# Performance work log

Hardware: AMD Instinct MI355X
Metric: run time of the kernel (lower is better)

Reference implementation:

```python
import jax, jax.numpy as jnp
import numpy as np

N_NODES = 100000


def _sage_conv(x, src, dst, W_l, b_l, W_r):
    # mean-aggregate neighbor (source) features at target nodes
    gathered = x[src]                                   # [E, D]
    summed = jax.ops.segment_sum(gathered, dst, num_segments=N_NODES)  # [N, D]
    deg = jax.ops.segment_sum(jnp.ones((src.shape[0],), x.dtype), dst,
                              num_segments=N_NODES)     # [N]
    mean = summed / jnp.maximum(deg, 1.0)[:, None]      # zero stays zero for isolated nodes
    # PyG SAGEConv: lin_l(aggr) + lin_r(x); bias on lin_l only
    return mean @ W_l + b_l + x @ W_r


def setup_inputs() -> dict:
    key = jax.random.key(0)
    ks = jax.random.split(key, 9)
    x = jax.random.normal(ks[0], (N_NODES, 128), dtype=jnp.float32)
    edge_index = jax.random.randint(ks[1], (2, 1600000), 0, N_NODES, dtype=jnp.int64)
    s1 = 1.0 / np.sqrt(128.0)
    s2 = 1.0 / np.sqrt(32.0)
    return {
        "x": x,
        "edge_index": edge_index,
        "W1_l": jax.random.normal(ks[2], (128, 32), jnp.float32) * s1,
        "b1_l": jax.random.normal(ks[3], (32,), jnp.float32) * s1,
        "W1_r": jax.random.normal(ks[4], (128, 32), jnp.float32) * s1,
        "W2_l": jax.random.normal(ks[5], (32, 32), jnp.float32) * s2,
        "b2_l": jax.random.normal(ks[6], (32,), jnp.float32) * s2,
        "W2_r": jax.random.normal(ks[7], (32, 32), jnp.float32) * s2,
    }


def reference(x, edge_index, W1_l, b1_l, W1_r, W2_l, b2_l, W2_r):
    src, dst = edge_index[0], edge_index[1]
    h = _sage_conv(x, src, dst, W1_l, b1_l, W1_r)
    h = jax.nn.relu(h)
    # dropout is identity in eval mode
    h = _sage_conv(h, src, dst, W2_l, b2_l, W2_r)
    return jax.nn.relu(h)
```

## Files before the change

kernel.cpp:

```cpp
#include <hip/hip_runtime.h>


typedef _Float16 f16;
typedef _Float16 f16x2 __attribute__((ext_vector_type(2)));
typedef _Float16 f16x4 __attribute__((ext_vector_type(4)));
typedef _Float16 half8 __attribute__((ext_vector_type(8)));
typedef float f32x4 __attribute__((ext_vector_type(4)));

#define MAXBINS 2048
#define SHIFT 6
#define BINSZ 64
#define CAP 48
#define BSTR 52
#define BC_SHIFT 11
#define GSC 256
#define BSC 512
#define SRC_BITS 17
#define SRC_MASK 0x1FFFFu
#define XSTRIDE 136


__global__ __launch_bounds__(256) void prep(const float* __restrict__ x,
                                            const float* __restrict__ Wl,
                                            const float* __restrict__ Wr,
                                            const int* __restrict__ dstIdx,
                                            int* __restrict__ blockHist,
                                            f16* __restrict__ yl,
                                            float* __restrict__ yr,
                                            int N, int E, int chunk, int gridG) {
    __shared__ __align__(16) f16 smem[2 * 64 * XSTRIDE];
    const int tid = threadIdx.x;

    if ((int)blockIdx.x >= gridG) {
        int* sh = (int*)smem;
        for (int i = tid; i < MAXBINS; i += 256) sh[i] = 0;
        __syncthreads();
        const int hb = blockIdx.x - gridG;
        const int base = hb * chunk;
        const int end = base + chunk < E ? base + chunk : E;
        if (base < E) {
            const int nv = (end - base) >> 2;
            const int4* d4 = (const int4*)(dstIdx + base);
            for (int i = tid; i < nv; i += 256) {
                int4 d = d4[i];
                atomicAdd(&sh[d.x >> SHIFT], 1);
                atomicAdd(&sh[d.y >> SHIFT], 1);
                atomicAdd(&sh[d.z >> SHIFT], 1);
                atomicAdd(&sh[d.w >> SHIFT], 1);
            }
            const int rem = (end - base) & 3;
            if (tid < rem) atomicAdd(&sh[dstIdx[base + nv * 4 + tid] >> SHIFT], 1);
        }
        __syncthreads();
        for (int i = tid; i < MAXBINS; i += 256)
            blockHist[(size_t)hb * MAXBINS + i] = sh[i];
        return;
    }

    f16* sX = smem;
    f16* sWT = smem + 64 * XSTRIDE;
    const int row0 = blockIdx.x * 64;

    for (int i = tid; i < 64 * 32; i += 256) {
        int r = i >> 5, c4 = i & 31;
        int row = row0 + r;
        float4 v = make_float4(0.f, 0.f, 0.f, 0.f);
        if (row < N) v = *(const float4*)(x + (size_t)row * 128 + c4 * 4);
        f16* d = &sX[r * XSTRIDE + c4 * 4];
        d[0] = (f16)v.x; d[1] = (f16)v.y; d[2] = (f16)v.z; d[3] = (f16)v.w;
    }
    for (int i = tid; i < 64 * 128; i += 256) {
        int k = i >> 6, n = i & 63;
        float v = (n < 32) ? Wl[k * 32 + n] : Wr[k * 32 + (n - 32)];
        sWT[n * XSTRIDE + k] = (f16)v;
    }
    __syncthreads();

    const int w = tid >> 6;
    const int lane = tid & 63;
    const int l15 = lane & 15, quad = lane >> 4;
    f32x4 acc[4] = {};
#pragma unroll
    for (int kc = 0; kc < 4; ++kc) {
        half8 af = *(const half8*)&sX[(w * 16 + l15) * XSTRIDE + kc * 32 + quad * 8];
#pragma unroll
        for (int nt = 0; nt < 4; ++nt) {
            half8 bf = *(const half8*)&sWT[(nt * 16 + l15) * XSTRIDE + kc * 32 + quad * 8];
            acc[nt] = __builtin_amdgcn_mfma_f32_16x16x32_f16(af, bf, acc[nt], 0, 0, 0);
        }
    }
#pragma unroll
    for (int nt = 0; nt < 4; ++nt) {
        int c = nt * 16 + l15;
#pragma unroll
        for (int r = 0; r < 4; ++r) {
            int g = row0 + w * 16 + quad * 4 + r;
            if (c < 32) yl[(size_t)g * 32 + c] = (f16)acc[nt][r];
            else        yr[(size_t)g * 32 + (c - 32)] = acc[nt][r];
        }
    }
}

__global__ __launch_bounds__(256) void col_scan(const int* __restrict__ blockHist,
                                                int* __restrict__ blockBaseRel,
                                                int* __restrict__ binCnt) {
    const int wave = threadIdx.x >> 6;
    const int lane = threadIdx.x & 63;
    const int bin = blockIdx.x * 4 + wave;
    int carry = 0;
#pragma unroll
    for (int r = 0; r < GSC / 64; ++r) {
        int b = r * 64 + lane;
        int v = blockHist[(size_t)b * MAXBINS + bin];
        int inc = v;
#pragma unroll
        for (int off = 1; off < 64; off <<= 1) {
            int t = __shfl_up(inc, off, 64);
            if (lane >= off) inc += t;
        }
        blockBaseRel[(size_t)b * MAXBINS + bin] = carry + (inc - v);
        carry += __shfl(inc, 63, 64);
    }
    binCnt[bin] = carry;
}

__global__ __launch_bounds__(BSC) void scatter_binned(const int* __restrict__ src,
                                                      const int* __restrict__ dst,
                                                      const int* __restrict__ blockBaseRel,
                                                      unsigned* __restrict__ pairs,
                                                      int E, int chunk) {
    __shared__ int cur[MAXBINS];
    for (int i = threadIdx.x; i < MAXBINS; i += BSC)
        cur[i] = blockBaseRel[(size_t)blockIdx.x * MAXBINS + i] + (i << BC_SHIFT);
    __syncthreads();
    const int base = blockIdx.x * chunk;
    const int end = base + chunk < E ? base + chunk : E;
    if (base >= E) return;
    const int nv = (end - base) >> 2;
    const int4* s4 = (const int4*)(src + base);
    const int4* d4 = (const int4*)(dst + base);
    for (int i = threadIdx.x; i < nv; i += BSC) {
        int4 s = s4[i];
        int4 d = d4[i];
        int slot;
        slot = atomicAdd(&cur[d.x >> SHIFT], 1);
        pairs[slot] = ((unsigned)(d.x & (BINSZ - 1)) << SRC_BITS) | (unsigned)s.x;
        slot = atomicAdd(&cur[d.y >> SHIFT], 1);
        pairs[slot] = ((unsigned)(d.y & (BINSZ - 1)) << SRC_BITS) | (unsigned)s.y;
        slot = atomicAdd(&cur[d.z >> SHIFT], 1);
        pairs[slot] = ((unsigned)(d.z & (BINSZ - 1)) << SRC_BITS) | (unsigned)s.z;
        slot = atomicAdd(&cur[d.w >> SHIFT], 1);
        pairs[slot] = ((unsigned)(d.w & (BINSZ - 1)) << SRC_BITS) | (unsigned)s.w;
    }
    const int rem = (end - base) & 3;
    if ((int)threadIdx.x < rem) {
        int e = base + nv * 4 + threadIdx.x;
        int s = src[e], d = dst[e];
        int slot = atomicAdd(&cur[d >> SHIFT], 1);
        pairs[slot] = ((unsigned)(d & (BINSZ - 1)) << SRC_BITS) | (unsigned)s;
    }
}


__global__ __launch_bounds__(256) void agg_l1(const unsigned* __restrict__ pairs,
                                              const int* __restrict__ binCnt,
                                              const f16* __restrict__ yl,
                                              const float* __restrict__ yr,
                                              const float* __restrict__ b1,
                                              const float* __restrict__ W2l,
                                              const float* __restrict__ W2r,
                                              f16* __restrict__ zl,
                                              float* __restrict__ zr,
                                              int N) {
    __shared__ __align__(16) int sBucket[BINSZ * BSTR];
    __shared__ int sCnt[BINSZ];
    __shared__ __align__(16) float sW[2048];
    __shared__ __align__(16) float sB[32];
    const int tid = threadIdx.x;
    if (tid < BINSZ) sCnt[tid] = 0;
    if (tid < 32) sB[tid] = b1[tid];
    {
        float4* sW4 = (float4*)sW;
        sW4[tid] = ((const float4*)W2l)[tid];
        sW4[256 + tid] = ((const float4*)W2r)[tid];
        for (int i = tid; i < BINSZ * BSTR; i += 256) sBucket[i] = N;
    }
    __syncthreads();

    const int b = blockIdx.x;
    const unsigned* pb = pairs + ((size_t)b << BC_SHIFT);
    const int cnt = binCnt[b];
    const int nv = cnt >> 2;
    const uint4* p4 = (const uint4*)pb;
    for (int i = tid; i < nv; i += 256) {
        uint4 pk = p4[i];
        int l, s;
        l = pk.x >> SRC_BITS; s = atomicAdd(&sCnt[l], 1);
        if (s < CAP) sBucket[l * BSTR + s] = (int)(pk.x & SRC_MASK);
        l = pk.y >> SRC_BITS; s = atomicAdd(&sCnt[l], 1);
        if (s < CAP) sBucket[l * BSTR + s] = (int)(pk.y & SRC_MASK);
        l = pk.z >> SRC_BITS; s = atomicAdd(&sCnt[l], 1);
        if (s < CAP) sBucket[l * BSTR + s] = (int)(pk.z & SRC_MASK);
        l = pk.w >> SRC_BITS; s = atomicAdd(&sCnt[l], 1);
        if (s < CAP) sBucket[l * BSTR + s] = (int)(pk.w & SRC_MASK);
    }
    {
        const int rem = cnt & 3;
        if (tid < rem) {
            unsigned pk = pb[nv * 4 + tid];
            int l = pk >> SRC_BITS;
            int s = atomicAdd(&sCnt[l], 1);
            if (s < CAP) sBucket[l * BSTR + s] = (int)(pk & SRC_MASK);
        }
    }
    __syncthreads();

    const int node = tid >> 2;
    const int c8 = tid & 3;
    const int node0 = b << SHIFT;
    const int g = node0 + node;

    const int deg = sCnt[node];
    const int m = deg < CAP ? deg : CAP;
    const int q = (m + 7) >> 3;
    const int4* bk = (const int4*)&sBucket[node * BSTR];
    const f16* yb = yl + c8 * 8;

    float ax[8] = {0.f, 0.f, 0.f, 0.f, 0.f, 0.f, 0.f, 0.f};
    for (int j = 0; j < q; ++j) {
        int4 eA = bk[2 * j];
        int4 eB = bk[2 * j + 1];
        half8 v0 = *(const half8*)(yb + (size_t)eA.x * 32);
        half8 v1 = *(const half8*)(yb + (size_t)eA.y * 32);
        half8 v2 = *(const half8*)(yb + (size_t)eA.z * 32);
        half8 v3 = *(const half8*)(yb + (size_t)eA.w * 32);
        half8 w0 = *(const half8*)(yb + (size_t)eB.x * 32);
        half8 w1 = *(const half8*)(yb + (size_t)eB.y * 32);
        half8 w2 = *(const half8*)(yb + (size_t)eB.z * 32);
        half8 w3 = *(const half8*)(yb + (size_t)eB.w * 32);
#pragma unroll
        for (int k = 0; k < 8; ++k)
            ax[k] += (((float)v0[k] + (float)v1[k]) + ((float)v2[k] + (float)v3[k]))
                   + (((float)w0[k] + (float)w1[k]) + ((float)w2[k] + (float)w3[k]));
    }

    float h[8];
    if (g < N) {
        float dg = deg > 1 ? (float)deg : 1.0f;
        float loc[8];
        *(float4*)&loc[0] = *(const float4*)(yr + (size_t)g * 32 + c8 * 8);
        *(float4*)&loc[4] = *(const float4*)(yr + (size_t)g * 32 + c8 * 8 + 4);
#pragma unroll
        for (int k = 0; k < 8; ++k)
            h[k] = fmaxf(ax[k] / dg + sB[c8 * 8 + k] + loc[k], 0.0f);
    } else {
#pragma unroll
        for (int k = 0; k < 8; ++k) h[k] = 0.f;
    }
    __syncthreads();

    float* sH = (float*)sBucket;
    *(float4*)&sH[node * 36 + c8 * 8]     = make_float4(h[0], h[1], h[2], h[3]);
    *(float4*)&sH[node * 36 + c8 * 8 + 4] = make_float4(h[4], h[5], h[6], h[7]);
    __syncthreads();

    const int n2 = tid >> 3;
    const int cq = tid & 7;
    const float4* sW4l = (const float4*)sW;
    const float4* sW4r = (const float4*)(sW + 1024);
#pragma unroll
    for (int it = 0; it < 2; ++it) {
        int n = it * 32 + n2;
        int gg = node0 + n;
        float4 al = make_float4(0.f, 0.f, 0.f, 0.f);
        float4 ar = make_float4(0.f, 0.f, 0.f, 0.f);
#pragma unroll 8
        for (int k = 0; k < 32; ++k) {
            float hk = sH[n * 36 + k];
            float4 wl = sW4l[k * 8 + cq];
            float4 wr = sW4r[k * 8 + cq];
            al.x += hk * wl.x; al.y += hk * wl.y; al.z += hk * wl.z; al.w += hk * wl.w;
            ar.x += hk * wr.x; ar.y += hk * wr.y; ar.z += hk * wr.z; ar.w += hk * wr.w;
        }
        f16x4 hh;
        hh[0] = (f16)al.x; hh[1] = (f16)al.y; hh[2] = (f16)al.z; hh[3] = (f16)al.w;
        *(f16x4*)(zl + (size_t)gg * 32 + cq * 4) = hh;
        if (gg < N) *(float4*)(zr + (size_t)gg * 32 + cq * 4) = ar;
    }
}

__global__ __launch_bounds__(256) void agg_l2(const unsigned* __restrict__ pairs,
                                              const int* __restrict__ binCnt,
                                              const f16* __restrict__ zl,
                                              const float* __restrict__ b2,
                                              float* __restrict__ io,
                                              int N) {
    __shared__ __align__(16) int sBucket[BINSZ * BSTR];
    __shared__ int sCnt[BINSZ];
    __shared__ __align__(16) float sB[32];
    const int tid = threadIdx.x;
    if (tid < BINSZ) sCnt[tid] = 0;
    if (tid < 32) sB[tid] = b2[tid];
    for (int i = tid; i < BINSZ * BSTR; i += 256) sBucket[i] = N;
    __syncthreads();

    const int b = blockIdx.x;
    const unsigned* pb = pairs + ((size_t)b << BC_SHIFT);
    const int cnt = binCnt[b];
    const int nv = cnt >> 2;
    const uint4* p4 = (const uint4*)pb;
    for (int i = tid; i < nv; i += 256) {
        uint4 pk = p4[i];
        int l, s;
        l = pk.x >> SRC_BITS; s = atomicAdd(&sCnt[l], 1);
        if (s < CAP) sBucket[l * BSTR + s] = (int)(pk.x & SRC_MASK);
        l = pk.y >> SRC_BITS; s = atomicAdd(&sCnt[l], 1);
        if (s < CAP) sBucket[l * BSTR + s] = (int)(pk.y & SRC_MASK);
        l = pk.z >> SRC_BITS; s = atomicAdd(&sCnt[l], 1);
        if (s < CAP) sBucket[l * BSTR + s] = (int)(pk.z & SRC_MASK);
        l = pk.w >> SRC_BITS; s = atomicAdd(&sCnt[l], 1);
        if (s < CAP) sBucket[l * BSTR + s] = (int)(pk.w & SRC_MASK);
    }
    {
        const int rem = cnt & 3;
        if (tid < rem) {
            unsigned pk = pb[nv * 4 + tid];
            int l = pk >> SRC_BITS;
            int s = atomicAdd(&sCnt[l], 1);
            if (s < CAP) sBucket[l * BSTR + s] = (int)(pk & SRC_MASK);
        }
    }
    __syncthreads();

    const int node = tid >> 2;
    const int c8 = tid & 3;
    const int node0 = b << SHIFT;
    const int g = node0 + node;

    const int deg = sCnt[node];
    const int m = deg < CAP ? deg : CAP;
    const int q = (m + 7) >> 3;
    const int4* bk = (const int4*)&sBucket[node * BSTR];
    const f16* zb = zl + c8 * 8;

    float ax[8] = {0.f, 0.f, 0.f, 0.f, 0.f, 0.f, 0.f, 0.f};
    for (int j = 0; j < q; ++j) {
        int4 eA = bk[2 * j];
        int4 eB = bk[2 * j + 1];
        half8 v0 = *(const half8*)(zb + (size_t)eA.x * 32);
        half8 v1 = *(const half8*)(zb + (size_t)eA.y * 32);
        half8 v2 = *(const half8*)(zb + (size_t)eA.z * 32);
        half8 v3 = *(const half8*)(zb + (size_t)eA.w * 32);
        half8 w0 = *(const half8*)(zb + (size_t)eB.x * 32);
        half8 w1 = *(const half8*)(zb + (size_t)eB.y * 32);
        half8 w2 = *(const half8*)(zb + (size_t)eB.z * 32);
        half8 w3 = *(const half8*)(zb + (size_t)eB.w * 32);
#pragma unroll
        for (int k = 0; k < 8; ++k)
            ax[k] += (((float)v0[k] + (float)v1[k]) + ((float)v2[k] + (float)v3[k]))
                   + (((float)w0[k] + (float)w1[k]) + ((float)w2[k] + (float)w3[k]));
    }

    if (g < N) {
        float dg = deg > 1 ? (float)deg : 1.0f;
        float v[8];
        *(float4*)&v[0] = *(const float4*)(io + (size_t)g * 32 + c8 * 8);
        *(float4*)&v[4] = *(const float4*)(io + (size_t)g * 32 + c8 * 8 + 4);
        float o[8];
#pragma unroll
        for (int k = 0; k < 8; ++k)
            o[k] = fmaxf(ax[k] / dg + sB[c8 * 8 + k] + v[k], 0.0f);
        *(float4*)(io + (size_t)g * 32 + c8 * 8)     = *(float4*)&o[0];
        *(float4*)(io + (size_t)g * 32 + c8 * 8 + 4) = *(float4*)&o[4];
    }
}

extern "C" void kernel_launch(void* const* d_in, const int* in_sizes, int n_in,
                              void* d_out, int out_size, void* d_ws, size_t ws_size,
                              hipStream_t stream) {
    const float* x    = (const float*)d_in[0];
    const int*   ei   = (const int*)d_in[1];
    const float* W1l  = (const float*)d_in[2];
    const float* b1l  = (const float*)d_in[3];
    const float* W1r  = (const float*)d_in[4];
    const float* W2l  = (const float*)d_in[5];
    const float* b2l  = (const float*)d_in[6];
    const float* W2r  = (const float*)d_in[7];

    const int N = in_sizes[0] / 128;
    const int E = in_sizes[1] / 2;
    const int* srcIdx = ei;
    const int* dstIdx = ei + E;

    const int gridG = (N >> 6) + 1;
    const int NP = gridG << 6;

    const int nbins = (N + BINSZ - 1) >> SHIFT;
    const int chunk = (((E + GSC - 1) / GSC) + 3) & ~3;

    int*      blockHist = (int*)d_ws;
    int*      blockBase = blockHist + (size_t)GSC * MAXBINS;
    int*      binCnt    = blockBase + (size_t)GSC * MAXBINS;
    unsigned* pairs     = (unsigned*)(binCnt + MAXBINS);
    f16*      A         = (f16*)(pairs + ((size_t)MAXBINS << BC_SHIFT));
    float*    B         = (float*)(A + (size_t)NP * 32);
    f16*      Z         = (f16*)(B + (size_t)NP * 32);
    float*    outp      = (float*)d_out;

    prep<<<gridG + GSC, 256, 0, stream>>>(x, W1l, W1r, dstIdx, blockHist,
                                          A, B, N, E, chunk, gridG);
    col_scan<<<MAXBINS / 4, 256, 0, stream>>>(blockHist, blockBase, binCnt);
    scatter_binned<<<GSC, BSC, 0, stream>>>(srcIdx, dstIdx, blockBase,
                                            pairs, E, chunk);
    agg_l1<<<nbins, 256, 0, stream>>>(pairs, binCnt, A, B, b1l,
                                      W2l, W2r, Z, outp, N);
    agg_l2<<<nbins, 256, 0, stream>>>(pairs, binCnt, Z, b2l, outp, N);
}
```

Baseline: 198.9 us.

## Cache per-bin bucketed adjacency from layer 1 for reuse in layer 2

agg_l1 now writes its shared-memory bucket table and per-node counts to a global workspace after building them. agg_l2 loads that table directly instead of re-reading the packed pairs and rebuilding buckets with shared atomics. The change also hoists the self-feature loads ahead of the gather loop and adds a min-blocks launch bound of 4. This trades extra global writes and reads of about 13.5KB per bin for removing the atomic bucketing work in layer 2.

```diff
diff --git a/kernel.cpp b/kernel.cpp
--- a/kernel.cpp
+++ b/kernel.cpp
@@ -2,7 +2,6 @@
 
 
 typedef _Float16 f16;
-typedef _Float16 f16x2 __attribute__((ext_vector_type(2)));
 typedef _Float16 f16x4 __attribute__((ext_vector_type(4)));
 typedef _Float16 half8 __attribute__((ext_vector_type(8)));
 typedef float f32x4 __attribute__((ext_vector_type(4)));
@@ -12,6 +11,7 @@
 #define BINSZ 64
 #define CAP 48
 #define BSTR 52
+#define GBI 3392
 #define BC_SHIFT 11
 #define GSC 256
 #define BSC 512
@@ -162,18 +162,38 @@
 }
 
 
-__global__ __launch_bounds__(256) void agg_l1(const unsigned* __restrict__ pairs,
-                                              const int* __restrict__ binCnt,
-                                              const f16* __restrict__ yl,
-                                              const float* __restrict__ yr,
-                                              const float* __restrict__ b1,
-                                              const float* __restrict__ W2l,
-                                              const float* __restrict__ W2r,
-                                              f16* __restrict__ zl,
-                                              float* __restrict__ zr,
-                                              int N) {
+#define PULL8(BKP, TBL, AX)                                                  \
+    {                                                                        \
+        int4 eA = (BKP)[0], eB = (BKP)[1];                                   \
+        half8 v0 = *(const half8*)((TBL) + (size_t)eA.x * 32);               \
+        half8 v1 = *(const half8*)((TBL) + (size_t)eA.y * 32);               \
+        half8 v2 = *(const half8*)((TBL) + (size_t)eA.z * 32);               \
+        half8 v3 = *(const half8*)((TBL) + (size_t)eA.w * 32);               \
+        half8 w0 = *(const half8*)((TBL) + (size_t)eB.x * 32);               \
+        half8 w1 = *(const half8*)((TBL) + (size_t)eB.y * 32);               \
+        half8 w2 = *(const half8*)((TBL) + (size_t)eB.z * 32);               \
+        half8 w3 = *(const half8*)((TBL) + (size_t)eB.w * 32);               \
+        _Pragma("unroll")                                                    \
+        for (int k_ = 0; k_ < 8; ++k_)                                       \
+            AX[k_] += (((float)v0[k_] + (float)v1[k_]) +                     \
+                       ((float)v2[k_] + (float)v3[k_])) +                    \
+                      (((float)w0[k_] + (float)w1[k_]) +                     \
+                       ((float)w2[k_] + (float)w3[k_]));                     \
+    }
+
+__global__ __launch_bounds__(256, 4) void agg_l1(const unsigned* __restrict__ pairs,
+                                                 const int* __restrict__ binCnt,
+                                                 int* __restrict__ gB,
+                                                 const f16* __restrict__ yl,
+                                                 const float* __restrict__ yr,
+                                                 const float* __restrict__ b1,
+                                                 const float* __restrict__ W2l,
+                                                 const float* __restrict__ W2r,
+                                                 f16* __restrict__ zl,
+                                                 float* __restrict__ zr,
+                                                 int N) {
     __shared__ __align__(16) int sBucket[BINSZ * BSTR];
-    __shared__ int sCnt[BINSZ];
+    __shared__ __align__(16) int sCnt[BINSZ];
     __shared__ __align__(16) float sW[2048];
     __shared__ __align__(16) float sB[32];
     const int tid = threadIdx.x;
@@ -188,23 +208,23 @@
     __syncthreads();
 
     const int b = blockIdx.x;
-    const unsigned* pb = pairs + ((size_t)b << BC_SHIFT);
-    const int cnt = binCnt[b];
-    const int nv = cnt >> 2;
-    const uint4* p4 = (const uint4*)pb;
-    for (int i = tid; i < nv; i += 256) {
-        uint4 pk = p4[i];
-        int l, s;
-        l = pk.x >> SRC_BITS; s = atomicAdd(&sCnt[l], 1);
-        if (s < CAP) sBucket[l * BSTR + s] = (int)(pk.x & SRC_MASK);
-        l = pk.y >> SRC_BITS; s = atomicAdd(&sCnt[l], 1);
-        if (s < CAP) sBucket[l * BSTR + s] = (int)(pk.y & SRC_MASK);
-        l = pk.z >> SRC_BITS; s = atomicAdd(&sCnt[l], 1);
-        if (s < CAP) sBucket[l * BSTR + s] = (int)(pk.z & SRC_MASK);
-        l = pk.w >> SRC_BITS; s = atomicAdd(&sCnt[l], 1);
-        if (s < CAP) sBucket[l * BSTR + s] = (int)(pk.w & SRC_MASK);
-    }
-    {
+    {
+        const unsigned* pb = pairs + ((size_t)b << BC_SHIFT);
+        const int cnt = binCnt[b];
+        const int nv = cnt >> 2;
+        const uint4* p4 = (const uint4*)pb;
+        for (int i = tid; i < nv; i += 256) {
+            uint4 pk = p4[i];
+            int l, s;
+            l = pk.x >> SRC_BITS; s = atomicAdd(&sCnt[l], 1);
+            if (s < CAP) sBucket[l * BSTR + s] = (int)(pk.x & SRC_MASK);
+            l = pk.y >> SRC_BITS; s = atomicAdd(&sCnt[l], 1);
+            if (s < CAP) sBucket[l * BSTR + s] = (int)(pk.y & SRC_MASK);
+            l = pk.z >> SRC_BITS; s = atomicAdd(&sCnt[l], 1);
+            if (s < CAP) sBucket[l * BSTR + s] = (int)(pk.z & SRC_MASK);
+            l = pk.w >> SRC_BITS; s = atomicAdd(&sCnt[l], 1);
+            if (s < CAP) sBucket[l * BSTR + s] = (int)(pk.w & SRC_MASK);
+        }
         const int rem = cnt & 3;
         if (tid < rem) {
             unsigned pk = pb[nv * 4 + tid];
@@ -215,41 +235,38 @@
     }
     __syncthreads();
 
+    {
+        int4* g4 = (int4*)(gB + (size_t)b * GBI);
+        const int4* s4 = (const int4*)sBucket;
+        for (int i = tid; i < 832; i += 256) g4[i] = s4[i];
+        if (tid < 16) g4[832 + tid] = ((const int4*)sCnt)[tid];
+    }
+
     const int node = tid >> 2;
     const int c8 = tid & 3;
     const int node0 = b << SHIFT;
     const int g = node0 + node;
 
-    const int deg = sCnt[node];
-    const int m = deg < CAP ? deg : CAP;
+    float4 locA = *(const float4*)(yr + (size_t)g * 32 + c8 * 8);
+    float4 locB = *(const float4*)(yr + (size_t)g * 32 + c8 * 8 + 4);
+
+    const int dgi = sCnt[node];
+    const int m = dgi < CAP ? dgi : CAP;
     const int q = (m + 7) >> 3;
     const int4* bk = (const int4*)&sBucket[node * BSTR];
-    const f16* yb = yl + c8 * 8;
+    const float dg = dgi > 1 ? (float)dgi : 1.0f;
 
     float ax[8] = {0.f, 0.f, 0.f, 0.f, 0.f, 0.f, 0.f, 0.f};
-    for (int j = 0; j < q; ++j) {
-        int4 eA = bk[2 * j];
-        int4 eB = bk[2 * j + 1];
-        half8 v0 = *(const half8*)(yb + (size_t)eA.x * 32);
-        half8 v1 = *(const half8*)(yb + (size_t)eA.y * 32);
-        half8 v2 = *(const half8*)(yb + (size_t)eA.z * 32);
-        half8 v3 = *(const half8*)(yb + (size_t)eA.w * 32);
-        half8 w0 = *(const half8*)(yb + (size_t)eB.x * 32);
-        half8 w1 = *(const half8*)(yb + (size_t)eB.y * 32);
-        half8 w2 = *(const half8*)(yb + (size_t)eB.z * 32);
-        half8 w3 = *(const half8*)(yb + (size_t)eB.w * 32);
-#pragma unroll
-        for (int k = 0; k < 8; ++k)
-            ax[k] += (((float)v0[k] + (float)v1[k]) + ((float)v2[k] + (float)v3[k]))
-                   + (((float)w0[k] + (float)w1[k]) + ((float)w2[k] + (float)w3[k]));
+    {
+        const f16* yb = yl + c8 * 8;
+        for (int j = 0; j < q; ++j) PULL8(bk + 2 * j, yb, ax);
     }
 
     float h[8];
     if (g < N) {
-        float dg = deg > 1 ? (float)deg : 1.0f;
         float loc[8];
-        *(float4*)&loc[0] = *(const float4*)(yr + (size_t)g * 32 + c8 * 8);
-        *(float4*)&loc[4] = *(const float4*)(yr + (size_t)g * 32 + c8 * 8 + 4);
+        *(float4*)&loc[0] = locA;
+        *(float4*)&loc[4] = locB;
 #pragma unroll
         for (int k = 0; k < 8; ++k)
             h[k] = fmaxf(ax[k] / dg + sB[c8 * 8 + k] + loc[k], 0.0f);
@@ -289,46 +306,23 @@
     }
 }
 
-__global__ __launch_bounds__(256) void agg_l2(const unsigned* __restrict__ pairs,
-                                              const int* __restrict__ binCnt,
-                                              const f16* __restrict__ zl,
-                                              const float* __restrict__ b2,
-                                              float* __restrict__ io,
-                                              int N) {
+__global__ __launch_bounds__(256, 4) void agg_l2(const int* __restrict__ gB,
+                                                 const f16* __restrict__ zl,
+                                                 const float* __restrict__ b2,
+                                                 float* __restrict__ io,
+                                                 int N) {
     __shared__ __align__(16) int sBucket[BINSZ * BSTR];
-    __shared__ int sCnt[BINSZ];
+    __shared__ __align__(16) int sCnt[BINSZ];
     __shared__ __align__(16) float sB[32];
     const int tid = threadIdx.x;
-    if (tid < BINSZ) sCnt[tid] = 0;
     if (tid < 32) sB[tid] = b2[tid];
-    for (int i = tid; i < BINSZ * BSTR; i += 256) sBucket[i] = N;
-    __syncthreads();
 
     const int b = blockIdx.x;
-    const unsigned* pb = pairs + ((size_t)b << BC_SHIFT);
-    const int cnt = binCnt[b];
-    const int nv = cnt >> 2;
-    const uint4* p4 = (const uint4*)pb;
-    for (int i = tid; i < nv; i += 256) {
-        uint4 pk = p4[i];
-        int l, s;
-        l = pk.x >> SRC_BITS; s = atomicAdd(&sCnt[l], 1);
-        if (s < CAP) sBucket[l * BSTR + s] = (int)(pk.x & SRC_MASK);
-        l = pk.y >> SRC_BITS; s = atomicAdd(&sCnt[l], 1);
-        if (s < CAP) sBucket[l * BSTR + s] = (int)(pk.y & SRC_MASK);
-        l = pk.z >> SRC_BITS; s = atomicAdd(&sCnt[l], 1);
-        if (s < CAP) sBucket[l * BSTR + s] = (int)(pk.z & SRC_MASK);
-        l = pk.w >> SRC_BITS; s = atomicAdd(&sCnt[l], 1);
-        if (s < CAP) sBucket[l * BSTR + s] = (int)(pk.w & SRC_MASK);
-    }
-    {
-        const int rem = cnt & 3;
-        if (tid < rem) {
-            unsigned pk = pb[nv * 4 + tid];
-            int l = pk >> SRC_BITS;
-            int s = atomicAdd(&sCnt[l], 1);
-            if (s < CAP) sBucket[l * BSTR + s] = (int)(pk & SRC_MASK);
-        }
+    {
+        const int4* g4 = (const int4*)(gB + (size_t)b * GBI);
+        int4* s4 = (int4*)sBucket;
+        for (int i = tid; i < 832; i += 256) s4[i] = g4[i];
+        if (tid < 16) ((int4*)sCnt)[tid] = g4[832 + tid];
     }
     __syncthreads();
 
@@ -337,35 +331,29 @@
     const int node0 = b << SHIFT;
     const int g = node0 + node;
 
-    const int deg = sCnt[node];
-    const int m = deg < CAP ? deg : CAP;
+    float4 ioA = make_float4(0.f, 0.f, 0.f, 0.f);
+    float4 ioB = make_float4(0.f, 0.f, 0.f, 0.f);
+    if (g < N) {
+        ioA = *(const float4*)(io + (size_t)g * 32 + c8 * 8);
+        ioB = *(const float4*)(io + (size_t)g * 32 + c8 * 8 + 4);
+    }
+
+    const int dgi = sCnt[node];
+    const int m = dgi < CAP ? dgi : CAP;
     const int q = (m + 7) >> 3;
     const int4* bk = (const int4*)&sBucket[node * BSTR];
-    const f16* zb = zl + c8 * 8;
 
     float ax[8] = {0.f, 0.f, 0.f, 0.f, 0.f, 0.f, 0.f, 0.f};
-    for (int j = 0; j < q; ++j) {
-        int4 eA = bk[2 * j];
-        int4 eB = bk[2 * j + 1];
-        half8 v0 = *(const half8*)(zb + (size_t)eA.x * 32);
-        half8 v1 = *(const half8*)(zb + (size_t)eA.y * 32);
-        half8 v2 = *(const half8*)(zb + (size_t)eA.z * 32);
-        half8 v3 = *(const half8*)(zb + (size_t)eA.w * 32);
-        half8 w0 = *(const half8*)(zb + (size_t)eB.x * 32);
-        half8 w1 = *(const half8*)(zb + (size_t)eB.y * 32);
-        half8 w2 = *(const half8*)(zb + (size_t)eB.z * 32);
-        half8 w3 = *(const half8*)(zb + (size_t)eB.w * 32);
-#pragma unroll
-        for (int k = 0; k < 8; ++k)
-            ax[k] += (((float)v0[k] + (float)v1[k]) + ((float)v2[k] + (float)v3[k]))
-                   + (((float)w0[k] + (float)w1[k]) + ((float)w2[k] + (float)w3[k]));
+    {
+        const f16* zb = zl + c8 * 8;
+        for (int j = 0; j < q; ++j) PULL8(bk + 2 * j, zb, ax);
     }
 
     if (g < N) {
-        float dg = deg > 1 ? (float)deg : 1.0f;
+        float dg = dgi > 1 ? (float)dgi : 1.0f;
         float v[8];
-        *(float4*)&v[0] = *(const float4*)(io + (size_t)g * 32 + c8 * 8);
-        *(float4*)&v[4] = *(const float4*)(io + (size_t)g * 32 + c8 * 8 + 4);
+        *(float4*)&v[0] = ioA;
+        *(float4*)&v[4] = ioB;
         float o[8];
 #pragma unroll
         for (int k = 0; k < 8; ++k)
@@ -405,6 +393,7 @@
     f16*      A         = (f16*)(pairs + ((size_t)MAXBINS << BC_SHIFT));
     float*    B         = (float*)(A + (size_t)NP * 32);
     f16*      Z         = (f16*)(B + (size_t)NP * 32);
+    int*      gB        = (int*)(Z + (size_t)NP * 32);
     float*    outp      = (float*)d_out;
 
     prep<<<gridG + GSC, 256, 0, stream>>>(x, W1l, W1r, dstIdx, blockHist,
@@ -412,7 +401,7 @@
     col_scan<<<MAXBINS / 4, 256, 0, stream>>>(blockHist, blockBase, binCnt);
     scatter_binned<<<GSC, BSC, 0, stream>>>(srcIdx, dstIdx, blockBase,
                                             pairs, E, chunk);
-    agg_l1<<<nbins, 256, 0, stream>>>(pairs, binCnt, A, B, b1l,
+    agg_l1<<<nbins, 256, 0, stream>>>(pairs, binCnt, gB, A, B, b1l,
                                       W2l, W2r, Z, outp, N);
-    agg_l2<<<nbins, 256, 0, stream>>>(pairs, binCnt, Z, b2l, outp, N);
-}
+    agg_l2<<<nbins, 256, 0, stream>>>(gB, Z, b2l, outp, N);
+}
```

Result: no change. 201.1 us (+1.1%).
